# Optimization experiments

Measured on AMD Instinct MI355X. Metric: run time of the kernel, lower is better.

Reference implementation:

```python
import jax, jax.numpy as jnp
import numpy as np
import math

B, S, E = 2, 2048, 1024
NH, NKV, HD = 16, 4, 64
GATE_CH = 12

def _rope(x, cos, sin):
    h = x.shape[-1] // 2
    x1, x2 = x[..., :h], x[..., h:]
    return jnp.concatenate((x1 * cos + x2 * sin, x1 * -sin + x2 * cos), axis=-1)

def _rms_norm(x):
    eps = jnp.finfo(x.dtype).eps
    return x * jax.lax.rsqrt(jnp.mean(x * x, axis=-1, keepdims=True) + eps)

def setup_inputs() -> dict:
    key = jax.random.key(0)
    ks = jax.random.split(key, 9)
    x = jax.random.normal(ks[0], (B, S, E), dtype=jnp.float32)
    ve = jax.random.normal(ks[1], (B, S, NKV * HD), dtype=jnp.float32)
    t = jnp.arange(S, dtype=jnp.float32)[:, None]
    inv_freq = 1.0 / (10000.0 ** (jnp.arange(0, HD // 2, dtype=jnp.float32) / (HD // 2)))
    ang = t * inv_freq[None, :]
    cos = jnp.cos(ang)[None, :, None, :]  # (1,S,1,HD//2)
    sin = jnp.sin(ang)[None, :, None, :]
    attn_mask = jnp.tril(jnp.ones((S, S), dtype=bool))[None, None]  # causal (1,1,S,S)
    sc = 0.02
    Wq = jax.random.normal(ks[2], (NH * HD, E), dtype=jnp.float32) * sc
    Wk = jax.random.normal(ks[3], (NKV * HD, E), dtype=jnp.float32) * sc
    Wv = jax.random.normal(ks[4], (NKV * HD, E), dtype=jnp.float32) * sc
    Wproj = jax.random.normal(ks[5], (E, E), dtype=jnp.float32) * sc
    Wgate = jax.random.normal(ks[6], (NKV, GATE_CH), dtype=jnp.float32) * sc
    return {"x": x, "ve": ve, "cos": cos, "sin": sin, "attn_mask": attn_mask,
            "Wq": Wq, "Wk": Wk, "Wv": Wv, "Wproj": Wproj, "Wgate": Wgate}

def reference(x, ve, cos, sin, attn_mask, Wq, Wk, Wv, Wproj, Wgate):
    b, s, _ = x.shape
    q = (x @ Wq.T).reshape(b, s, NH, HD)
    k = (x @ Wk.T).reshape(b, s, NKV, HD)
    v = (x @ Wv.T).reshape(b, s, NKV, HD)
    # value-embedding gating
    gate = 3.0 * jax.nn.sigmoid(x[..., :GATE_CH] @ Wgate.T)  # (b,s,NKV)
    v = v + gate[..., None] * ve.reshape(b, s, NKV, HD)
    # RoPE + QK-RMSNorm
    q = _rms_norm(_rope(q, cos, sin)) * 1.2
    k = _rms_norm(_rope(k, cos, sin)) * 1.2
    # GQA: repeat KV heads
    rep = NH // NKV
    k = jnp.repeat(k, rep, axis=2)
    v = jnp.repeat(v, rep, axis=2)
    q = q.transpose(0, 2, 1, 3)  # (b,h,s,d)
    k = k.transpose(0, 2, 1, 3)
    v = v.transpose(0, 2, 1, 3)
    scores = jnp.einsum('bhqd,bhkd->bhqk', q, k) / math.sqrt(HD)
    scores = jnp.where(attn_mask, scores, jnp.finfo(scores.dtype).min)
    attn = jax.nn.softmax(scores, axis=-1)
    y = jnp.einsum('bhqk,bhkd->bhqd', attn, v)
    y = y.transpose(0, 2, 1, 3).reshape(b, s, NH * HD)
    return y @ Wproj.T
```

## Files before the change

### kernel.cpp

```cpp
#include <hip/hip_runtime.h>
#include <hip/hip_bf16.h>
#include <math.h>

typedef short bf16x8 __attribute__((ext_vector_type(8)));
typedef float f32x4 __attribute__((ext_vector_type(4)));

#define LROW 72

__device__ __forceinline__ unsigned short f2bf(float f) {
  union { float f; unsigned int u; } v; v.f = f;
  unsigned int u = v.u;
  unsigned int r = (u + 0x7fffu + ((u >> 16) & 1u)) >> 16;
  return (unsigned short)r;
}
__device__ __forceinline__ float bf2f(unsigned short u) {
  return __uint_as_float((unsigned)u << 16);
}

#if __has_builtin(__builtin_amdgcn_global_load_lds)
#define HAVE_GLD 1
__device__ __forceinline__ void gld16(const void* g, void* l) {
  __builtin_amdgcn_global_load_lds(
      (const __attribute__((address_space(1))) unsigned int*)g,
      (__attribute__((address_space(3))) unsigned int*)l, 16, 0, 0);
}
#else
#define HAVE_GLD 0
#endif

__global__ __launch_bounds__(256) void cvt_all_kernel(const float* __restrict__ x,
                                                      const float* __restrict__ Wq,
                                                      const float* __restrict__ Wk,
                                                      const float* __restrict__ Wv,
                                                      const float* __restrict__ Wproj,
                                                      unsigned short* __restrict__ xb,
                                                      unsigned short* __restrict__ wqkv,
                                                      unsigned short* __restrict__ wpj) {
  int blk = blockIdx.x;
  const float* src;
  unsigned short* dst;
  if (blk < 4096)      { src = x + (size_t)blk * 1024;            dst = xb + (size_t)blk * 1024; }
  else if (blk < 5120) { src = Wq + (size_t)(blk - 4096) * 1024;  dst = wqkv + (size_t)(blk - 4096) * 1024; }
  else if (blk < 5376) { src = Wk + (size_t)(blk - 5120) * 1024;  dst = wqkv + (size_t)(blk - 4096) * 1024; }
  else if (blk < 5632) { src = Wv + (size_t)(blk - 5376) * 1024;  dst = wqkv + (size_t)(blk - 4096) * 1024; }
  else                 { src = Wproj + (size_t)(blk - 5632) * 1024; dst = wpj + (size_t)(blk - 5632) * 1024; }
  int i = threadIdx.x;
  float4 v = ((const float4*)src)[i];
  ushort4 o;
  o.x = f2bf(v.x); o.y = f2bf(v.y); o.z = f2bf(v.z); o.w = f2bf(v.w);
  ((ushort4*)dst)[i] = o;
}

__global__ __launch_bounds__(256) void gemm_qkv_kernel(const unsigned short* __restrict__ A,
                                                       const unsigned short* __restrict__ B,
                                                       const float* __restrict__ ve,
                                                       const float* __restrict__ cosb,
                                                       const float* __restrict__ sinb,
                                                       const float* __restrict__ wgate,
                                                       unsigned short* __restrict__ Q,
                                                       unsigned short* __restrict__ Kd,
                                                       unsigned short* __restrict__ Vt) {
  __shared__ unsigned short As[64 * 64];
  __shared__ unsigned short Bs[128 * 64];
  __shared__ float gLDS[128];
  const int K = 1024;
  int tid = threadIdx.x;
  int wave = tid >> 6, lane = tid & 63, l15 = lane & 15, quad = lane >> 4;
  int wm = (wave >> 1) * 32, wn = (wave & 1) * 64;
  int n0 = blockIdx.x * 128, m0 = blockIdx.y * 64;
  if (n0 >= 1280 && tid < 128) {
    int rl = tid & 63, khl = tid >> 6;
    int kh = ((n0 >> 6) - 20) + khl;
    float dot = 0.f;
#pragma unroll
    for (int jj = 0; jj < 12; jj++)
      dot += bf2f(A[(size_t)(m0 + rl) * 1024 + jj]) * wgate[kh * 12 + jj];
    gLDS[khl * 64 + rl] = 3.0f / (1.0f + __expf(-dot));
  }
  f32x4 acc[2][4];
#pragma unroll
  for (int i = 0; i < 2; i++)
#pragma unroll
    for (int j = 0; j < 4; j++) acc[i][j] = (f32x4){0.f, 0.f, 0.f, 0.f};
  int srow = lane >> 3;
  int scol = ((lane & 7) ^ srow) * 8;
  for (int k0 = 0; k0 < K; k0 += 64) {
    __syncthreads();
#if HAVE_GLD
#pragma unroll
    for (int j = 0; j < 2; j++) {
      int row = wave * 16 + j * 8;
      gld16(A + (size_t)(m0 + row + srow) * K + k0 + scol, As + row * 64 + lane * 8);
    }
#pragma unroll
    for (int j = 0; j < 4; j++) {
      int row = wave * 32 + j * 8;
      gld16(B + (size_t)(n0 + row + srow) * K + k0 + scol, Bs + row * 64 + lane * 8);
    }
#else
#pragma unroll
    for (int j = 0; j < 2; j++) {
      int row = wave * 16 + j * 8;
      *(float4*)(As + row * 64 + lane * 8) = *(const float4*)(A + (size_t)(m0 + row + srow) * K + k0 + scol);
    }
#pragma unroll
    for (int j = 0; j < 4; j++) {
      int row = wave * 32 + j * 8;
      *(float4*)(Bs + row * 64 + lane * 8) = *(const float4*)(B + (size_t)(n0 + row + srow) * K + k0 + scol);
    }
#endif
    __syncthreads();
#pragma unroll
    for (int s = 0; s < 2; s++) {
      bf16x8 af[2], bf[4];
#pragma unroll
      for (int i = 0; i < 2; i++)
        af[i] = *(const bf16x8*)(As + (wm + i * 16 + l15) * 64 + (((s * 4 + quad) ^ (l15 & 7)) * 8));
#pragma unroll
      for (int j = 0; j < 4; j++)
        bf[j] = *(const bf16x8*)(Bs + (wn + j * 16 + l15) * 64 + (((s * 4 + quad) ^ (l15 & 7)) * 8));
#pragma unroll
      for (int i = 0; i < 2; i++)
#pragma unroll
        for (int j = 0; j < 4; j++)
          acc[i][j] = __builtin_amdgcn_mfma_f32_16x16x32_bf16(af[i], bf[j], acc[i][j], 0, 0, 0);
    }
  }
  int hs = (n0 + wn) >> 6;
  if (hs < 20) {
    bool isq = hs < 16;
    float postscale = isq ? 0.216404256f : 1.2f;
#pragma unroll
    for (int i = 0; i < 2; i++) {
#pragma unroll
      for (int r = 0; r < 4; r++) {
        int row = m0 + wm + i * 16 + quad * 4 + r;
        int s = row & 2047, b = row >> 11;
        float c0 = cosb[s * 32 + l15],      s0 = sinb[s * 32 + l15];
        float c1 = cosb[s * 32 + 16 + l15], s1 = sinb[s * 32 + 16 + l15];
        float v0 = acc[i][0][r], v1 = acc[i][1][r], v2 = acc[i][2][r], v3 = acc[i][3][r];
        float n0v = fmaf(v0, c0,  v2 * s0);
        float n1v = fmaf(v1, c1,  v3 * s1);
        float n2v = fmaf(v2, c0, -v0 * s0);
        float n3v = fmaf(v3, c1, -v1 * s1);
        float ss = (n0v * n0v + n1v * n1v) + (n2v * n2v + n3v * n3v);
        ss += __shfl_xor(ss, 1, 64); ss += __shfl_xor(ss, 2, 64);
        ss += __shfl_xor(ss, 4, 64); ss += __shfl_xor(ss, 8, 64);
        float sc = rsqrtf(ss * (1.0f / 64.0f) + 1.1920929e-07f) * postscale;
        unsigned short* dp = isq ? Q + ((size_t)(b * 16 + hs) * 2048 + s) * 64
                                 : Kd + ((size_t)(b * 4 + hs - 16) * 2048 + s) * 64;
        dp[l15]      = f2bf(n0v * sc);
        dp[16 + l15] = f2bf(n1v * sc);
        dp[32 + l15] = f2bf(n2v * sc);
        dp[48 + l15] = f2bf(n3v * sc);
      }
    }
  } else {
    int kh = hs - 20;
#pragma unroll
    for (int i = 0; i < 2; i++) {
#pragma unroll
      for (int r = 0; r < 4; r++) {
        int rl = wm + i * 16 + quad * 4 + r;
        int row = m0 + rl, s = row & 2047, b = row >> 11;
        float g = gLDS[(wave & 1) * 64 + rl];
        const float* vep = ve + (size_t)row * 256 + kh * 64;
        unsigned short* vp = Vt + ((size_t)(b * 4 + kh) * 64) * 2048 + s;
#pragma unroll
        for (int j = 0; j < 4; j++) {
          float vv = fmaf(g, vep[j * 16 + l15], acc[i][j][r]);
          vp[(size_t)(j * 16 + l15) * 2048] = f2bf(vv);
        }
      }
    }
  }
}

__global__ __launch_bounds__(256) void flash_kernel(const unsigned short* __restrict__ Q,
                                                    const unsigned short* __restrict__ K,
                                                    const unsigned short* __restrict__ Vt,
                                                    unsigned short* __restrict__ Y) {
  __shared__ unsigned short Ks[64 * 64];
  __shared__ unsigned short Vs[64 * 64];
  __shared__ unsigned short Ps[4 * 16 * LROW];
  int pair = blockIdx.x, h = blockIdx.y, b = blockIdx.z;
  int hb = b * 16 + h;
  int kh = h >> 2;
  int tid = threadIdx.x, wave = tid >> 6, lane = tid & 63, l15 = lane & 15, quad = lane >> 4;
  int l7 = l15 & 7;
  const unsigned short* Kg = K + (size_t)(b * 4 + kh) * 2048 * 64;
  const unsigned short* Vg = Vt + (size_t)(b * 4 + kh) * 64 * 2048;
  unsigned short* Pw = Ps + wave * 16 * LROW;
  int row0 = tid >> 3, col8 = (tid & 7) * 8;
  int dchunk = (((tid & 7) ^ (row0 & 7)) * 8);

#pragma unroll
  for (int half = 0; half < 2; half++) {
    int qt = (half == 0) ? pair : 31 - pair;
    int NT = qt + 1;
    int q0 = qt * 64;
    const unsigned short* Qp = Q + (((size_t)hb * 2048) + q0 + wave * 16 + l15) * 64;
    bf16x8 qf0 = *(const bf16x8*)(Qp + quad * 8);
    bf16x8 qf1 = *(const bf16x8*)(Qp + 32 + quad * 8);
    f32x4 acc[4];
#pragma unroll
    for (int i = 0; i < 4; i++) acc[i] = (f32x4){0.f, 0.f, 0.f, 0.f};
    float l_lane = 0.f;

    {
      float4 pk0 = *(const float4*)(Kg + (size_t)row0 * 64 + col8);
      float4 pk1 = *(const float4*)(Kg + (size_t)(row0 + 32) * 64 + col8);
      float4 pv0 = *(const float4*)(Vg + (size_t)row0 * 2048 + col8);
      float4 pv1 = *(const float4*)(Vg + (size_t)(row0 + 32) * 2048 + col8);

      for (int kt = 0; kt < NT; kt++) {
        int k0 = kt * 64;
        __syncthreads();
        *(float4*)(Ks + row0 * 64 + dchunk) = pk0;
        *(float4*)(Ks + (row0 + 32) * 64 + dchunk) = pk1;
        *(float4*)(Vs + row0 * 64 + dchunk) = pv0;
        *(float4*)(Vs + (row0 + 32) * 64 + dchunk) = pv1;
        if (kt + 1 < NT) {
          int kn = k0 + 64;
          pk0 = *(const float4*)(Kg + (size_t)(kn + row0) * 64 + col8);
          pk1 = *(const float4*)(Kg + (size_t)(kn + row0 + 32) * 64 + col8);
          pv0 = *(const float4*)(Vg + (size_t)row0 * 2048 + kn + col8);
          pv1 = *(const float4*)(Vg + (size_t)(row0 + 32) * 2048 + kn + col8);
        }
        __syncthreads();

        f32x4 sv[4];
        __builtin_amdgcn_s_setprio(1);
#pragma unroll
        for (int mt = 0; mt < 4; mt++) {
          sv[mt] = (f32x4){0.f, 0.f, 0.f, 0.f};
          bf16x8 k0f = *(const bf16x8*)(Ks + (mt * 16 + l15) * 64 + ((quad ^ l7) * 8));
          sv[mt] = __builtin_amdgcn_mfma_f32_16x16x32_bf16(k0f, qf0, sv[mt], 0, 0, 0);
          bf16x8 k1f = *(const bf16x8*)(Ks + (mt * 16 + l15) * 64 + (((4 + quad) ^ l7) * 8));
          sv[mt] = __builtin_amdgcn_mfma_f32_16x16x32_bf16(k1f, qf1, sv[mt], 0, 0, 0);
        }
        __builtin_amdgcn_s_setprio(0);
        if (kt == qt) {
          int qg = q0 + wave * 16 + l15;
#pragma unroll
          for (int mt = 0; mt < 4; mt++) {
            int kg = k0 + mt * 16 + quad * 4;
#pragma unroll
            for (int r = 0; r < 4; r++)
              if (kg + r > qg) sv[mt][r] = -1e30f;
          }
        }
#pragma unroll
        for (int mt = 0; mt < 4; mt++) {
          float p0 = __builtin_amdgcn_exp2f(sv[mt][0]);
          float p1 = __builtin_amdgcn_exp2f(sv[mt][1]);
          float p2 = __builtin_amdgcn_exp2f(sv[mt][2]);
          float p3 = __builtin_amdgcn_exp2f(sv[mt][3]);
          l_lane += (p0 + p1) + (p2 + p3);
          unsigned int lo = __builtin_amdgcn_perm(__float_as_uint(p1), __float_as_uint(p0), 0x07060302u);
          unsigned int hi = __builtin_amdgcn_perm(__float_as_uint(p3), __float_as_uint(p2), 0x07060302u);
          *(uint2*)(Pw + l15 * LROW + mt * 16 + quad * 4) = make_uint2(lo, hi);
        }
        __builtin_amdgcn_s_setprio(1);
#pragma unroll
        for (int step = 0; step < 2; step++) {
          bf16x8 pa = *(const bf16x8*)(Pw + l15 * LROW + step * 32 + quad * 8);
#pragma unroll
          for (int nt = 0; nt < 4; nt++) {
            bf16x8 vb = *(const bf16x8*)(Vs + (nt * 16 + l15) * 64 + (((step * 4 + quad) ^ l7) * 8));
            acc[nt] = __builtin_amdgcn_mfma_f32_16x16x32_bf16(pa, vb, acc[nt], 0, 0, 0);
          }
        }
        __builtin_amdgcn_s_setprio(0);
      }
    }
    l_lane += __shfl_xor(l_lane, 16, 64);
    l_lane += __shfl_xor(l_lane, 32, 64);

#pragma unroll
    for (int r = 0; r < 4; r++) {
      float inv = 1.0f / __shfl(l_lane, quad * 4 + r, 16);
      int qrow = q0 + wave * 16 + quad * 4 + r;
      unsigned short* yp = Y + ((size_t)(b * 2048 + qrow) * 1024) + h * 64;
#pragma unroll
      for (int nt = 0; nt < 4; nt++)
        yp[nt * 16 + l15] = f2bf(acc[nt][r] * inv);
    }
  }
}

__global__ __launch_bounds__(256) void gemm_proj_kernel(const unsigned short* __restrict__ A,
                                                        const unsigned short* __restrict__ B,
                                                        float* __restrict__ C) {
  __shared__ unsigned short As[128 * 64];
  __shared__ unsigned short Bs[64 * 64];
  const int K = 1024, N = 1024;
  int tid = threadIdx.x;
  int wave = tid >> 6, lane = tid & 63, l15 = lane & 15, quad = lane >> 4;
  int wm = (wave >> 1) * 64, wn = (wave & 1) * 32;
  int n0 = blockIdx.x * 64, m0 = blockIdx.y * 128;
  f32x4 acc[4][2];
#pragma unroll
  for (int i = 0; i < 4; i++)
#pragma unroll
    for (int j = 0; j < 2; j++) acc[i][j] = (f32x4){0.f, 0.f, 0.f, 0.f};
  int srow = lane >> 3;
  int scol = ((lane & 7) ^ srow) * 8;
  for (int k0 = 0; k0 < K; k0 += 64) {
    __syncthreads();
#if HAVE_GLD
#pragma unroll
    for (int j = 0; j < 4; j++) {
      int row = wave * 32 + j * 8;
      gld16(A + (size_t)(m0 + row + srow) * K + k0 + scol, As + row * 64 + lane * 8);
    }
#pragma unroll
    for (int j = 0; j < 2; j++) {
      int row = wave * 16 + j * 8;
      gld16(B + (size_t)(n0 + row + srow) * K + k0 + scol, Bs + row * 64 + lane * 8);
    }
#else
#pragma unroll
    for (int j = 0; j < 4; j++) {
      int row = wave * 32 + j * 8;
      *(float4*)(As + row * 64 + lane * 8) = *(const float4*)(A + (size_t)(m0 + row + srow) * K + k0 + scol);
    }
#pragma unroll
    for (int j = 0; j < 2; j++) {
      int row = wave * 16 + j * 8;
      *(float4*)(Bs + row * 64 + lane * 8) = *(const float4*)(B + (size_t)(n0 + row + srow) * K + k0 + scol);
    }
#endif
    __syncthreads();
#pragma unroll
    for (int s = 0; s < 2; s++) {
      bf16x8 af[4], bf[2];
#pragma unroll
      for (int i = 0; i < 4; i++)
        af[i] = *(const bf16x8*)(As + (wm + i * 16 + l15) * 64 + (((s * 4 + quad) ^ (l15 & 7)) * 8));
#pragma unroll
      for (int j = 0; j < 2; j++)
        bf[j] = *(const bf16x8*)(Bs + (wn + j * 16 + l15) * 64 + (((s * 4 + quad) ^ (l15 & 7)) * 8));
#pragma unroll
      for (int i = 0; i < 4; i++)
#pragma unroll
        for (int j = 0; j < 2; j++)
          acc[i][j] = __builtin_amdgcn_mfma_f32_16x16x32_bf16(af[i], bf[j], acc[i][j], 0, 0, 0);
    }
  }
#pragma unroll
  for (int i = 0; i < 4; i++)
#pragma unroll
    for (int j = 0; j < 2; j++)
#pragma unroll
      for (int r = 0; r < 4; r++)
        C[(size_t)(m0 + wm + i * 16 + quad * 4 + r) * N + n0 + wn + j * 16 + l15] = acc[i][j][r];
}

extern "C" void kernel_launch(void* const* d_in, const int* in_sizes, int n_in,
                              void* d_out, int out_size, void* d_ws, size_t ws_size,
                              hipStream_t stream) {
  const float* x     = (const float*)d_in[0];
  const float* ve    = (const float*)d_in[1];
  const float* cosb  = (const float*)d_in[2];
  const float* sinb  = (const float*)d_in[3];
  const float* Wq    = (const float*)d_in[5];
  const float* Wk    = (const float*)d_in[6];
  const float* Wv    = (const float*)d_in[7];
  const float* Wproj = (const float*)d_in[8];
  const float* Wgate = (const float*)d_in[9];
  float* out = (float*)d_out;
  char* ws = (char*)d_ws;

  size_t o = 0;
  unsigned short* xb   = (unsigned short*)(ws + o); o += (size_t)4096 * 1024 * 2;
  unsigned short* wqkv = (unsigned short*)(ws + o); o += (size_t)1536 * 1024 * 2;
  unsigned short* wpj  = (unsigned short*)(ws + o); o += (size_t)1024 * 1024 * 2;
  unsigned short* Qb   = (unsigned short*)(ws + o); o += (size_t)2 * 16 * 2048 * 64 * 2;
  unsigned short* Kb   = (unsigned short*)(ws + o); o += (size_t)2 * 4 * 2048 * 64 * 2;
  unsigned short* Vb   = (unsigned short*)(ws + o); o += (size_t)2 * 4 * 2048 * 64 * 2;
  unsigned short* Yb   = (unsigned short*)(ws + o); o += (size_t)4096 * 1024 * 2;

  hipLaunchKernelGGL(cvt_all_kernel, dim3(6656), dim3(256), 0, stream,
                     x, Wq, Wk, Wv, Wproj, xb, wqkv, wpj);
  hipLaunchKernelGGL(gemm_qkv_kernel, dim3(12, 64), dim3(256), 0, stream,
                     xb, wqkv, ve, cosb, sinb, Wgate, Qb, Kb, Vb);
  hipLaunchKernelGGL(flash_kernel, dim3(16, 16, 2), dim3(256), 0, stream,
                     Qb, Kb, Vb, Yb);
  hipLaunchKernelGGL(gemm_proj_kernel, dim3(16, 32), dim3(256), 0, stream, Yb, wpj, out);
}
```

Before: 173.6 us.

## Double-buffer LDS tiles in QKV and projection GEMMs, enlarge proj tile

Both GEMM kernels now keep two LDS buffers and prefetch the next K-slice while MFMAs run on the current one, dropping one barrier per iteration. This is meant to hide global-load latency behind compute. The projection GEMM also grows its block tile from 128x64 to 128x128, giving each wave 4x4 accumulators and more reuse per LDS load. The cost is a 256-block grid instead of 512 on a large-CU GPU, plus more LDS and registers per block, which can lower occupancy.

```diff
diff --git a/kernel.cpp b/kernel.cpp
--- a/kernel.cpp
+++ b/kernel.cpp
@@ -60,8 +60,8 @@
                                                        unsigned short* __restrict__ Q,
                                                        unsigned short* __restrict__ Kd,
                                                        unsigned short* __restrict__ Vt) {
-  __shared__ unsigned short As[64 * 64];
-  __shared__ unsigned short Bs[128 * 64];
+  __shared__ unsigned short As[2][64 * 64];
+  __shared__ unsigned short Bs[2][128 * 64];
   __shared__ float gLDS[128];
   const int K = 1024;
   int tid = threadIdx.x;
@@ -84,47 +84,77 @@
     for (int j = 0; j < 4; j++) acc[i][j] = (f32x4){0.f, 0.f, 0.f, 0.f};
   int srow = lane >> 3;
   int scol = ((lane & 7) ^ srow) * 8;
+
+#if HAVE_GLD
+#pragma unroll
+  for (int j = 0; j < 2; j++) {
+    int row = wave * 16 + j * 8;
+    gld16(A + (size_t)(m0 + row + srow) * K + scol, As[0] + row * 64 + lane * 8);
+  }
+#pragma unroll
+  for (int j = 0; j < 4; j++) {
+    int row = wave * 32 + j * 8;
+    gld16(B + (size_t)(n0 + row + srow) * K + scol, Bs[0] + row * 64 + lane * 8);
+  }
+#else
+#pragma unroll
+  for (int j = 0; j < 2; j++) {
+    int row = wave * 16 + j * 8;
+    *(float4*)(As[0] + row * 64 + lane * 8) = *(const float4*)(A + (size_t)(m0 + row + srow) * K + scol);
+  }
+#pragma unroll
+  for (int j = 0; j < 4; j++) {
+    int row = wave * 32 + j * 8;
+    *(float4*)(Bs[0] + row * 64 + lane * 8) = *(const float4*)(B + (size_t)(n0 + row + srow) * K + scol);
+  }
+#endif
+  __syncthreads();
+
   for (int k0 = 0; k0 < K; k0 += 64) {
-    __syncthreads();
+    int cur = (k0 >> 6) & 1;
+    const unsigned short* Ac = As[cur];
+    const unsigned short* Bc = Bs[cur];
+    if (k0 + 64 < K) {
 #if HAVE_GLD
 #pragma unroll
-    for (int j = 0; j < 2; j++) {
-      int row = wave * 16 + j * 8;
-      gld16(A + (size_t)(m0 + row + srow) * K + k0 + scol, As + row * 64 + lane * 8);
-    }
-#pragma unroll
-    for (int j = 0; j < 4; j++) {
-      int row = wave * 32 + j * 8;
-      gld16(B + (size_t)(n0 + row + srow) * K + k0 + scol, Bs + row * 64 + lane * 8);
-    }
+      for (int j = 0; j < 2; j++) {
+        int row = wave * 16 + j * 8;
+        gld16(A + (size_t)(m0 + row + srow) * K + k0 + 64 + scol, As[cur ^ 1] + row * 64 + lane * 8);
+      }
+#pragma unroll
+      for (int j = 0; j < 4; j++) {
+        int row = wave * 32 + j * 8;
+        gld16(B + (size_t)(n0 + row + srow) * K + k0 + 64 + scol, Bs[cur ^ 1] + row * 64 + lane * 8);
+      }
 #else
 #pragma unroll
-    for (int j = 0; j < 2; j++) {
-      int row = wave * 16 + j * 8;
-      *(float4*)(As + row * 64 + lane * 8) = *(const float4*)(A + (size_t)(m0 + row + srow) * K + k0 + scol);
-    }
-#pragma unroll
-    for (int j = 0; j < 4; j++) {
-      int row = wave * 32 + j * 8;
-      *(float4*)(Bs + row * 64 + lane * 8) = *(const float4*)(B + (size_t)(n0 + row + srow) * K + k0 + scol);
-    }
+      for (int j = 0; j < 2; j++) {
+        int row = wave * 16 + j * 8;
+        *(float4*)(As[cur ^ 1] + row * 64 + lane * 8) = *(const float4*)(A + (size_t)(m0 + row + srow) * K + k0 + 64 + scol);
+      }
+#pragma unroll
+      for (int j = 0; j < 4; j++) {
+        int row = wave * 32 + j * 8;
+        *(float4*)(Bs[cur ^ 1] + row * 64 + lane * 8) = *(const float4*)(B + (size_t)(n0 + row + srow) * K + k0 + 64 + scol);
+      }
 #endif
-    __syncthreads();
+    }
 #pragma unroll
     for (int s = 0; s < 2; s++) {
       bf16x8 af[2], bf[4];
 #pragma unroll
       for (int i = 0; i < 2; i++)
-        af[i] = *(const bf16x8*)(As + (wm + i * 16 + l15) * 64 + (((s * 4 + quad) ^ (l15 & 7)) * 8));
+        af[i] = *(const bf16x8*)(Ac + (wm + i * 16 + l15) * 64 + (((s * 4 + quad) ^ (l15 & 7)) * 8));
 #pragma unroll
       for (int j = 0; j < 4; j++)
-        bf[j] = *(const bf16x8*)(Bs + (wn + j * 16 + l15) * 64 + (((s * 4 + quad) ^ (l15 & 7)) * 8));
+        bf[j] = *(const bf16x8*)(Bc + (wn + j * 16 + l15) * 64 + (((s * 4 + quad) ^ (l15 & 7)) * 8));
 #pragma unroll
       for (int i = 0; i < 2; i++)
 #pragma unroll
         for (int j = 0; j < 4; j++)
           acc[i][j] = __builtin_amdgcn_mfma_f32_16x16x32_bf16(af[i], bf[j], acc[i][j], 0, 0, 0);
     }
+    __syncthreads();
   }
   int hs = (n0 + wn) >> 6;
   if (hs < 20) {
@@ -292,69 +322,83 @@
 __global__ __launch_bounds__(256) void gemm_proj_kernel(const unsigned short* __restrict__ A,
                                                         const unsigned short* __restrict__ B,
                                                         float* __restrict__ C) {
-  __shared__ unsigned short As[128 * 64];
-  __shared__ unsigned short Bs[64 * 64];
+  __shared__ unsigned short As[2][128 * 64];
+  __shared__ unsigned short Bs[2][128 * 64];
   const int K = 1024, N = 1024;
   int tid = threadIdx.x;
   int wave = tid >> 6, lane = tid & 63, l15 = lane & 15, quad = lane >> 4;
-  int wm = (wave >> 1) * 64, wn = (wave & 1) * 32;
-  int n0 = blockIdx.x * 64, m0 = blockIdx.y * 128;
-  f32x4 acc[4][2];
+  int wr = (wave >> 1) * 64, wc = (wave & 1) * 64;
+  int n0 = blockIdx.x * 128, m0 = blockIdx.y * 128;
+  f32x4 acc[4][4];
 #pragma unroll
   for (int i = 0; i < 4; i++)
 #pragma unroll
-    for (int j = 0; j < 2; j++) acc[i][j] = (f32x4){0.f, 0.f, 0.f, 0.f};
+    for (int j = 0; j < 4; j++) acc[i][j] = (f32x4){0.f, 0.f, 0.f, 0.f};
   int srow = lane >> 3;
   int scol = ((lane & 7) ^ srow) * 8;
+
+#if HAVE_GLD
+#pragma unroll
+  for (int j = 0; j < 4; j++) {
+    int row = wave * 32 + j * 8;
+    gld16(A + (size_t)(m0 + row + srow) * K + scol, As[0] + row * 64 + lane * 8);
+    gld16(B + (size_t)(n0 + row + srow) * K + scol, Bs[0] + row * 64 + lane * 8);
+  }
+#else
+#pragma unroll
+  for (int j = 0; j < 4; j++) {
+    int row = wave * 32 + j * 8;
+    *(float4*)(As[0] + row * 64 + lane * 8) = *(const float4*)(A + (size_t)(m0 + row + srow) * K + scol);
+    *(float4*)(Bs[0] + row * 64 + lane * 8) = *(const float4*)(B + (size_t)(n0 + row + srow) * K + scol);
+  }
+#endif
+  __syncthreads();
+
   for (int k0 = 0; k0 < K; k0 += 64) {
+    int cur = (k0 >> 6) & 1;
+    const unsigned short* Ac = As[cur];
+    const unsigned short* Bc = Bs[cur];
+    if (k0 + 64 < K) {
+#if HAVE_GLD
+#pragma unroll
+      for (int j = 0; j < 4; j++) {
+        int row = wave * 32 + j * 8;
+        gld16(A + (size_t)(m0 + row + srow) * K + k0 + 64 + scol, As[cur ^ 1] + row * 64 + lane * 8);
+        gld16(B + (size_t)(n0 + row + srow) * K + k0 + 64 + scol, Bs[cur ^ 1] + row * 64 + lane * 8);
+      }
+#else
+#pragma unroll
+      for (int j = 0; j < 4; j++) {
+        int row = wave * 32 + j * 8;
+        *(float4*)(As[cur ^ 1] + row * 64 + lane * 8) = *(const float4*)(A + (size_t)(m0 + row + srow) * K + k0 + 64 + scol);
+        *(float4*)(Bs[cur ^ 1] + row * 64 + lane * 8) = *(const float4*)(B + (size_t)(n0 + row + srow) * K + k0 + 64 + scol);
+      }
+#endif
+    }
+#pragma unroll
+    for (int s = 0; s < 2; s++) {
+      bf16x8 af[4], bf[4];
+#pragma unroll
+      for (int i = 0; i < 4; i++)
+        af[i] = *(const bf16x8*)(Ac + (wr + i * 16 + l15) * 64 + (((s * 4 + quad) ^ (l15 & 7)) * 8));
+#pragma unroll
+      for (int j = 0; j < 4; j++)
+        bf[j] = *(const bf16x8*)(Bc + (wc + j * 16 + l15) * 64 + (((s * 4 + quad) ^ (l15 & 7)) * 8));
+#pragma unroll
+      for (int i = 0; i < 4; i++)
+#pragma unroll
+        for (int j = 0; j < 4; j++)
+          acc[i][j] = __builtin_amdgcn_mfma_f32_16x16x32_bf16(af[i], bf[j], acc[i][j], 0, 0, 0);
+    }
     __syncthreads();
-#if HAVE_GLD
-#pragma unroll
-    for (int j = 0; j < 4; j++) {
-      int row = wave * 32 + j * 8;
-      gld16(A + (size_t)(m0 + row + srow) * K + k0 + scol, As + row * 64 + lane * 8);
-    }
-#pragma unroll
-    for (int j = 0; j < 2; j++) {
-      int row = wave * 16 + j * 8;
-      gld16(B + (size_t)(n0 + row + srow) * K + k0 + scol, Bs + row * 64 + lane * 8);
-    }
-#else
-#pragma unroll
-    for (int j = 0; j < 4; j++) {
-      int row = wave * 32 + j * 8;
-      *(float4*)(As + row * 64 + lane * 8) = *(const float4*)(A + (size_t)(m0 + row + srow) * K + k0 + scol);
-    }
-#pragma unroll
-    for (int j = 0; j < 2; j++) {
-      int row = wave * 16 + j * 8;
-      *(float4*)(Bs + row * 64 + lane * 8) = *(const float4*)(B + (size_t)(n0 + row + srow) * K + k0 + scol);
-    }
-#endif
-    __syncthreads();
-#pragma unroll
-    for (int s = 0; s < 2; s++) {
-      bf16x8 af[4], bf[2];
-#pragma unroll
-      for (int i = 0; i < 4; i++)
-        af[i] = *(const bf16x8*)(As + (wm + i * 16 + l15) * 64 + (((s * 4 + quad) ^ (l15 & 7)) * 8));
-#pragma unroll
-      for (int j = 0; j < 2; j++)
-        bf[j] = *(const bf16x8*)(Bs + (wn + j * 16 + l15) * 64 + (((s * 4 + quad) ^ (l15 & 7)) * 8));
-#pragma unroll
-      for (int i = 0; i < 4; i++)
-#pragma unroll
-        for (int j = 0; j < 2; j++)
-          acc[i][j] = __builtin_amdgcn_mfma_f32_16x16x32_bf16(af[i], bf[j], acc[i][j], 0, 0, 0);
-    }
   }
 #pragma unroll
   for (int i = 0; i < 4; i++)
 #pragma unroll
-    for (int j = 0; j < 2; j++)
+    for (int j = 0; j < 4; j++)
 #pragma unroll
       for (int r = 0; r < 4; r++)
-        C[(size_t)(m0 + wm + i * 16 + quad * 4 + r) * N + n0 + wn + j * 16 + l15] = acc[i][j][r];
+        C[(size_t)(m0 + wr + i * 16 + quad * 4 + r) * N + n0 + wc + j * 16 + l15] = acc[i][j][r];
 }
 
 extern "C" void kernel_launch(void* const* d_in, const int* in_sizes, int n_in,
@@ -387,5 +431,5 @@
                      xb, wqkv, ve, cosb, sinb, Wgate, Qb, Kb, Vb);
   hipLaunchKernelGGL(flash_kernel, dim3(16, 16, 2), dim3(256), 0, stream,
                      Qb, Kb, Vb, Yb);
-  hipLaunchKernelGGL(gemm_proj_kernel, dim3(16, 32), dim3(256), 0, stream, Yb, wpj, out);
-}
+  hipLaunchKernelGGL(gemm_proj_kernel, dim3(8, 32), dim3(256), 0, stream, Yb, wpj, out);
+}
```

Measured after the change: 179.5 us. +3.4%, slower.

## Load K and V fragments directly from global memory in flash kernel

Applied to the files above, without the earlier changes.

Removes the shared-memory staging of K and V tiles, their register prefetch and both block barriers per key tile. Each wave now reads its MFMA operands straight from global memory, relying on L1/L2 caching for reuse across the four waves. This drops synchronisation and LDS traffic, but each tile is fetched four times through the cache and global-load latency is no longer hidden by the register double-buffer.

```diff
diff --git a/kernel.cpp b/kernel.cpp
--- a/kernel.cpp
+++ b/kernel.cpp
@@ -180,19 +180,14 @@
                                                     const unsigned short* __restrict__ K,
                                                     const unsigned short* __restrict__ Vt,
                                                     unsigned short* __restrict__ Y) {
-  __shared__ unsigned short Ks[64 * 64];
-  __shared__ unsigned short Vs[64 * 64];
   __shared__ unsigned short Ps[4 * 16 * LROW];
   int pair = blockIdx.x, h = blockIdx.y, b = blockIdx.z;
   int hb = b * 16 + h;
   int kh = h >> 2;
   int tid = threadIdx.x, wave = tid >> 6, lane = tid & 63, l15 = lane & 15, quad = lane >> 4;
-  int l7 = l15 & 7;
   const unsigned short* Kg = K + (size_t)(b * 4 + kh) * 2048 * 64;
   const unsigned short* Vg = Vt + (size_t)(b * 4 + kh) * 64 * 2048;
   unsigned short* Pw = Ps + wave * 16 * LROW;
-  int row0 = tid >> 3, col8 = (tid & 7) * 8;
-  int dchunk = (((tid & 7) ^ (row0 & 7)) * 8);
 
 #pragma unroll
   for (int half = 0; half < 2; half++) {
@@ -207,72 +202,52 @@
     for (int i = 0; i < 4; i++) acc[i] = (f32x4){0.f, 0.f, 0.f, 0.f};
     float l_lane = 0.f;
 
-    {
-      float4 pk0 = *(const float4*)(Kg + (size_t)row0 * 64 + col8);
-      float4 pk1 = *(const float4*)(Kg + (size_t)(row0 + 32) * 64 + col8);
-      float4 pv0 = *(const float4*)(Vg + (size_t)row0 * 2048 + col8);
-      float4 pv1 = *(const float4*)(Vg + (size_t)(row0 + 32) * 2048 + col8);
-
-      for (int kt = 0; kt < NT; kt++) {
-        int k0 = kt * 64;
-        __syncthreads();
-        *(float4*)(Ks + row0 * 64 + dchunk) = pk0;
-        *(float4*)(Ks + (row0 + 32) * 64 + dchunk) = pk1;
-        *(float4*)(Vs + row0 * 64 + dchunk) = pv0;
-        *(float4*)(Vs + (row0 + 32) * 64 + dchunk) = pv1;
-        if (kt + 1 < NT) {
-          int kn = k0 + 64;
-          pk0 = *(const float4*)(Kg + (size_t)(kn + row0) * 64 + col8);
-          pk1 = *(const float4*)(Kg + (size_t)(kn + row0 + 32) * 64 + col8);
-          pv0 = *(const float4*)(Vg + (size_t)row0 * 2048 + kn + col8);
-          pv1 = *(const float4*)(Vg + (size_t)(row0 + 32) * 2048 + kn + col8);
+    for (int kt = 0; kt < NT; kt++) {
+      int k0 = kt * 64;
+      f32x4 sv[4];
+      __builtin_amdgcn_s_setprio(1);
+#pragma unroll
+      for (int mt = 0; mt < 4; mt++) {
+        const unsigned short* kr = Kg + (size_t)(k0 + mt * 16 + l15) * 64;
+        sv[mt] = (f32x4){0.f, 0.f, 0.f, 0.f};
+        bf16x8 k0f = *(const bf16x8*)(kr + quad * 8);
+        sv[mt] = __builtin_amdgcn_mfma_f32_16x16x32_bf16(k0f, qf0, sv[mt], 0, 0, 0);
+        bf16x8 k1f = *(const bf16x8*)(kr + 32 + quad * 8);
+        sv[mt] = __builtin_amdgcn_mfma_f32_16x16x32_bf16(k1f, qf1, sv[mt], 0, 0, 0);
+      }
+      __builtin_amdgcn_s_setprio(0);
+      if (kt == qt) {
+        int qg = q0 + wave * 16 + l15;
+#pragma unroll
+        for (int mt = 0; mt < 4; mt++) {
+          int kg = k0 + mt * 16 + quad * 4;
+#pragma unroll
+          for (int r = 0; r < 4; r++)
+            if (kg + r > qg) sv[mt][r] = -1e30f;
         }
-        __syncthreads();
-
-        f32x4 sv[4];
-        __builtin_amdgcn_s_setprio(1);
-#pragma unroll
-        for (int mt = 0; mt < 4; mt++) {
-          sv[mt] = (f32x4){0.f, 0.f, 0.f, 0.f};
-          bf16x8 k0f = *(const bf16x8*)(Ks + (mt * 16 + l15) * 64 + ((quad ^ l7) * 8));
-          sv[mt] = __builtin_amdgcn_mfma_f32_16x16x32_bf16(k0f, qf0, sv[mt], 0, 0, 0);
-          bf16x8 k1f = *(const bf16x8*)(Ks + (mt * 16 + l15) * 64 + (((4 + quad) ^ l7) * 8));
-          sv[mt] = __builtin_amdgcn_mfma_f32_16x16x32_bf16(k1f, qf1, sv[mt], 0, 0, 0);
+      }
+#pragma unroll
+      for (int mt = 0; mt < 4; mt++) {
+        float p0 = __builtin_amdgcn_exp2f(sv[mt][0]);
+        float p1 = __builtin_amdgcn_exp2f(sv[mt][1]);
+        float p2 = __builtin_amdgcn_exp2f(sv[mt][2]);
+        float p3 = __builtin_amdgcn_exp2f(sv[mt][3]);
+        l_lane += (p0 + p1) + (p2 + p3);
+        unsigned int lo = __builtin_amdgcn_perm(__float_as_uint(p1), __float_as_uint(p0), 0x07060302u);
+        unsigned int hi = __builtin_amdgcn_perm(__float_as_uint(p3), __float_as_uint(p2), 0x07060302u);
+        *(uint2*)(Pw + l15 * LROW + mt * 16 + quad * 4) = make_uint2(lo, hi);
+      }
+      __builtin_amdgcn_s_setprio(1);
+#pragma unroll
+      for (int step = 0; step < 2; step++) {
+        bf16x8 pa = *(const bf16x8*)(Pw + l15 * LROW + step * 32 + quad * 8);
+#pragma unroll
+        for (int nt = 0; nt < 4; nt++) {
+          bf16x8 vb = *(const bf16x8*)(Vg + (size_t)(nt * 16 + l15) * 2048 + k0 + (step * 4 + quad) * 8);
+          acc[nt] = __builtin_amdgcn_mfma_f32_16x16x32_bf16(pa, vb, acc[nt], 0, 0, 0);
         }
-        __builtin_amdgcn_s_setprio(0);
-        if (kt == qt) {
-          int qg = q0 + wave * 16 + l15;
-#pragma unroll
-          for (int mt = 0; mt < 4; mt++) {
-            int kg = k0 + mt * 16 + quad * 4;
-#pragma unroll
-            for (int r = 0; r < 4; r++)
-              if (kg + r > qg) sv[mt][r] = -1e30f;
-          }
-        }
-#pragma unroll
-        for (int mt = 0; mt < 4; mt++) {
-          float p0 = __builtin_amdgcn_exp2f(sv[mt][0]);
-          float p1 = __builtin_amdgcn_exp2f(sv[mt][1]);
-          float p2 = __builtin_amdgcn_exp2f(sv[mt][2]);
-          float p3 = __builtin_amdgcn_exp2f(sv[mt][3]);
-          l_lane += (p0 + p1) + (p2 + p3);
-          unsigned int lo = __builtin_amdgcn_perm(__float_as_uint(p1), __float_as_uint(p0), 0x07060302u);
-          unsigned int hi = __builtin_amdgcn_perm(__float_as_uint(p3), __float_as_uint(p2), 0x07060302u);
-          *(uint2*)(Pw + l15 * LROW + mt * 16 + quad * 4) = make_uint2(lo, hi);
-        }
-        __builtin_amdgcn_s_setprio(1);
-#pragma unroll
-        for (int step = 0; step < 2; step++) {
-          bf16x8 pa = *(const bf16x8*)(Pw + l15 * LROW + step * 32 + quad * 8);
-#pragma unroll
-          for (int nt = 0; nt < 4; nt++) {
-            bf16x8 vb = *(const bf16x8*)(Vs + (nt * 16 + l15) * 64 + (((step * 4 + quad) ^ l7) * 8));
-            acc[nt] = __builtin_amdgcn_mfma_f32_16x16x32_bf16(pa, vb, acc[nt], 0, 0, 0);
-          }
-        }
-        __builtin_amdgcn_s_setprio(0);
-      }
+      }
+      __builtin_amdgcn_s_setprio(0);
     }
     l_lane += __shfl_xor(l_lane, 16, 64);
     l_lane += __shfl_xor(l_lane, 32, 64);
```

Result: slower. 259.7 us (+49.6%).
